# Optimization experiments

Measured on AMD Instinct MI355X. Metric: run time of the kernel, lower is better.

The kernel has to match this reference:

```python
import jax, jax.numpy as jnp
import numpy as np

N_NODES = 100000
IN_DIM = 128
HIDDEN = 64
N_EDGES = 1600000


def setup_inputs() -> dict:
    key = jax.random.key(0)
    k_z, k_e, k_w1, k_b1, k_w2, k_b2 = jax.random.split(key, 6)
    z = jax.random.normal(k_z, (N_NODES, IN_DIM), dtype=jnp.float32)
    edge_index = jax.random.randint(k_e, (2, N_EDGES), 0, N_NODES, dtype=jnp.int64)
    # PyTorch Linear stores weight [out, in]; keep [in, out] layout for x @ W
    bound1 = 1.0 / np.sqrt(2 * IN_DIM)
    W1 = jax.random.uniform(k_w1, (2 * IN_DIM, HIDDEN), jnp.float32, -bound1, bound1)
    b1 = jax.random.uniform(k_b1, (HIDDEN,), jnp.float32, -bound1, bound1)
    bound2 = 1.0 / np.sqrt(HIDDEN)
    W2 = jax.random.uniform(k_w2, (HIDDEN, 1), jnp.float32, -bound2, bound2)
    b2 = jax.random.uniform(k_b2, (1,), jnp.float32, -bound2, bound2)
    return {"z": z, "edge_index": edge_index, "W1": W1, "b1": b1, "W2": W2, "b2": b2}


def reference(z, edge_index, W1, b1, W2, b2):
    src = edge_index[0]
    dst = edge_index[1]
    # gather node features and concat: [E, 2*D]
    edge_feat = jnp.concatenate([z[src], z[dst]], axis=-1)
    h = jax.nn.relu(edge_feat @ W1 + b1)  # [E, H]
    logits = h @ W2 + b2                  # [E, 1]
    return jax.nn.sigmoid(logits).squeeze(-1)  # [E]
```

## Files before the change

kernel.cpp:

```cpp
#include <hip/hip_runtime.h>
#include <hip/hip_bf16.h>

#define N_NODES 100000
#define IN_DIM  128
#define HIDDEN  64
#define N_EDGES 1600000

typedef unsigned short u16;
typedef unsigned int   u32;

typedef __attribute__((ext_vector_type(8))) short bf16x8;
typedef __attribute__((ext_vector_type(4))) float f32x4;

__device__ __forceinline__ u16 f2bf(float f) {
    u32 u = __float_as_uint(f);
    u32 r = 0x7FFFu + ((u >> 16) & 1u);
    u += r;
    return (u16)(u >> 16);
}

__global__ __launch_bounds__(256) void prep_kernel(const float* __restrict__ W1,
                                                   u16* __restrict__ WcatT) {
    int idx = blockIdx.x * 256 + threadIdx.x;
    int jj = idx >> 7;
    int k  = idx & 127;
    float v = (jj < 64) ? W1[k * 64 + jj] : W1[(128 + k) * 64 + (jj - 64)];
    WcatT[idx] = f2bf(v);
}

#define LDK 136
#define GEMM_BLOCKS 625

__global__ __launch_bounds__(256) void gemm_kernel(const float* __restrict__ z,
                                                   const u16* __restrict__ WcatT,
                                                   const float* __restrict__ b1,
                                                   u16* __restrict__ UV) {
    __shared__ u16 Bs[128 * LDK];

    int tid = threadIdx.x;
    for (int c = tid; c < 128 * 16; c += 256) {
        int row = c >> 4, cc = c & 15;
        *(uint4*)(Bs + row * LDK + cc * 8) = *(const uint4*)(WcatT + row * 128 + cc * 8);
    }
    __syncthreads();

    int wave = tid >> 6;
    int lane = tid & 63;
    int quad = lane >> 4;
    int l16  = lane & 15;

    int gwid   = blockIdx.x * 4 + wave;
    int nwaves = GEMM_BLOCKS * 4;
    const int NTILES = N_NODES / 16;

    float bias[4];
#pragma unroll
    for (int nt = 0; nt < 4; nt++) bias[nt] = b1[nt * 16 + l16];

    for (int t = gwid; t < NTILES; t += nwaves) {
        const float* zrow = z + (size_t)(t * 16 + l16) * 128;

        float4 fa[8];
#pragma unroll
        for (int kb = 0; kb < 4; kb++) {
            fa[kb * 2]     = *(const float4*)(zrow + kb * 32 + quad * 8);
            fa[kb * 2 + 1] = *(const float4*)(zrow + kb * 32 + quad * 8 + 4);
        }
        bf16x8 afrag[4];
#pragma unroll
        for (int kb = 0; kb < 4; kb++) {
            union { bf16x8 v; u32 w[4]; } pk;
            float4 lo = fa[kb * 2], hi = fa[kb * 2 + 1];
            pk.w[0] = (u32)f2bf(lo.x) | ((u32)f2bf(lo.y) << 16);
            pk.w[1] = (u32)f2bf(lo.z) | ((u32)f2bf(lo.w) << 16);
            pk.w[2] = (u32)f2bf(hi.x) | ((u32)f2bf(hi.y) << 16);
            pk.w[3] = (u32)f2bf(hi.z) | ((u32)f2bf(hi.w) << 16);
            afrag[kb] = pk.v;
        }

        f32x4 acc[8];
        const f32x4 z4 = {0.f, 0.f, 0.f, 0.f};
#pragma unroll
        for (int i = 0; i < 8; i++) acc[i] = z4;

#pragma unroll
        for (int kb = 0; kb < 4; kb++) {
            int k0 = kb * 32 + quad * 8;
#pragma unroll
            for (int nt = 0; nt < 8; nt++) {
                bf16x8 b = *(const bf16x8*)(Bs + (nt * 16 + l16) * LDK + k0);
                acc[nt] = __builtin_amdgcn_mfma_f32_16x16x32_bf16(afrag[kb], b, acc[nt], 0, 0, 0);
            }
        }

#pragma unroll
        for (int nt = 0; nt < 8; nt++) {
            float bb = (nt < 4) ? bias[nt] : 0.f;
#pragma unroll
            for (int r = 0; r < 4; r++) {
                int row = t * 16 + quad * 4 + r;
                UV[(size_t)row * 128 + nt * 16 + l16] = f2bf(acc[nt][r] + bb);
            }
        }
    }
}

#define EDGE_ITERS 8
#define BATCH 4

__global__ __launch_bounds__(256) void edge_kernel(const int* __restrict__ ei,
                                                   const u16* __restrict__ UV,
                                                   const float* __restrict__ W2,
                                                   const float* __restrict__ b2,
                                                   float* __restrict__ out) {
    int gwave = (blockIdx.x * 256 + threadIdx.x) >> 6;
    int lane  = threadIdx.x & 63;
    int sub   = lane >> 3;
    int c     = lane & 7;

    float4 w2a = *(const float4*)(W2 + c * 8);
    float4 w2b = *(const float4*)(W2 + c * 8 + 4);
    float w2r[8] = {w2a.x, w2a.y, w2a.z, w2a.w, w2b.x, w2b.y, w2b.z, w2b.w};
    float b2v = b2[0];

    int ebase = gwave * (8 * EDGE_ITERS) + sub;

#pragma unroll
    for (int it4 = 0; it4 < EDGE_ITERS; it4 += BATCH) {
        int sB[BATCH], dB[BATCH];
#pragma unroll
        for (int j = 0; j < BATCH; j++) {
            int e = ebase + (it4 + j) * 8;
            sB[j] = ei[e];
            dB[j] = ei[N_EDGES + e];
        }
        uint4 aB[BATCH], bB[BATCH];
#pragma unroll
        for (int j = 0; j < BATCH; j++) {
            aB[j] = *(const uint4*)(UV + (size_t)sB[j] * 128 + c * 8);
            bB[j] = *(const uint4*)(UV + (size_t)dB[j] * 128 + 64 + c * 8);
        }
#pragma unroll
        for (int j = 0; j < BATCH; j++) {
            u32 aw[4] = {aB[j].x, aB[j].y, aB[j].z, aB[j].w};
            u32 bw[4] = {bB[j].x, bB[j].y, bB[j].z, bB[j].w};
            float acc = 0.f;
#pragma unroll
            for (int i = 0; i < 4; i++) {
                float u0 = __uint_as_float(aw[i] << 16);
                float u1 = __uint_as_float(aw[i] & 0xFFFF0000u);
                float v0 = __uint_as_float(bw[i] << 16);
                float v1 = __uint_as_float(bw[i] & 0xFFFF0000u);
                float h0 = fmaxf(u0 + v0, 0.f);
                float h1 = fmaxf(u1 + v1, 0.f);
                acc = fmaf(h0, w2r[i * 2], acc);
                acc = fmaf(h1, w2r[i * 2 + 1], acc);
            }
            acc += __shfl_xor(acc, 1);
            acc += __shfl_xor(acc, 2);
            acc += __shfl_xor(acc, 4);
            if (c == 0) {
                int e = ebase + (it4 + j) * 8;
                float x = acc + b2v;
                out[e] = 1.f / (1.f + __expf(-x));
            }
        }
    }
}

extern "C" void kernel_launch(void* const* d_in, const int* in_sizes, int n_in,
                              void* d_out, int out_size, void* d_ws, size_t ws_size,
                              hipStream_t stream) {
    const float* z  = (const float*)d_in[0];
    const int*   ei = (const int*)d_in[1];
    const float* W1 = (const float*)d_in[2];
    const float* b1 = (const float*)d_in[3];
    const float* W2 = (const float*)d_in[4];
    const float* b2 = (const float*)d_in[5];
    float* out = (float*)d_out;

    u16* WcatT = (u16*)d_ws;
    u16* UV    = (u16*)((char*)d_ws + 65536);

    prep_kernel<<<64, 256, 0, stream>>>(W1, WcatT);
    gemm_kernel<<<GEMM_BLOCKS, 256, 0, stream>>>(z, WcatT, b1, UV);
    edge_kernel<<<6250, 256, 0, stream>>>(ei, UV, W2, b2, out);
}
```

Baseline: 164.2 us.

## Store per-node projections as FP8 and batch all edge gathers up front

The GEMM now writes the projected node features U/V as FP8 (e4m3 via hardware pack conversion) instead of bf16. This halves the intermediate buffer and the random-gather traffic in the edge kernel. The edge kernel issues all 8 edges' index and feature loads before computing, with a scheduling barrier, nontemporal index loads and stores, and a launch-bounds occupancy hint. FP8 quantization adds noticeable error in the hidden activations, which could exceed the accuracy tolerance.

After: 151.6 us. 7.7% less time.

```diff
diff --git a/kernel.cpp b/kernel.cpp
--- a/kernel.cpp
+++ b/kernel.cpp
@@ -8,15 +8,22 @@
 
 typedef unsigned short u16;
 typedef unsigned int   u32;
+typedef unsigned char  u8;
 
 typedef __attribute__((ext_vector_type(8))) short bf16x8;
 typedef __attribute__((ext_vector_type(4))) float f32x4;
+typedef __attribute__((ext_vector_type(2))) float f32x2;
 
 __device__ __forceinline__ u16 f2bf(float f) {
     u32 u = __float_as_uint(f);
     u32 r = 0x7FFFu + ((u >> 16) & 1u);
     u += r;
     return (u16)(u >> 16);
+}
+
+__device__ __forceinline__ u8 f2fp8(float f) {
+    u32 p = (u32)__builtin_amdgcn_cvt_pk_fp8_f32(f, f, 0, false);
+    return (u8)(p & 0xFF);
 }
 
 __global__ __launch_bounds__(256) void prep_kernel(const float* __restrict__ W1,
@@ -34,7 +41,7 @@
 __global__ __launch_bounds__(256) void gemm_kernel(const float* __restrict__ z,
                                                    const u16* __restrict__ WcatT,
                                                    const float* __restrict__ b1,
-                                                   u16* __restrict__ UV) {
+                                                   u8* __restrict__ UVq) {
     __shared__ u16 Bs[128 * LDK];
 
     int tid = threadIdx.x;
@@ -99,20 +106,19 @@
 #pragma unroll
             for (int r = 0; r < 4; r++) {
                 int row = t * 16 + quad * 4 + r;
-                UV[(size_t)row * 128 + nt * 16 + l16] = f2bf(acc[nt][r] + bb);
+                UVq[(size_t)row * 128 + nt * 16 + l16] = f2fp8(acc[nt][r] + bb);
             }
         }
     }
 }
 
-#define EDGE_ITERS 8
-#define BATCH 4
+#define BATCH 8
 
-__global__ __launch_bounds__(256) void edge_kernel(const int* __restrict__ ei,
-                                                   const u16* __restrict__ UV,
-                                                   const float* __restrict__ W2,
-                                                   const float* __restrict__ b2,
-                                                   float* __restrict__ out) {
+__global__ __launch_bounds__(256, 2) void edge_kernel(const int* __restrict__ ei,
+                                                      const u8* __restrict__ UVq,
+                                                      const float* __restrict__ W2,
+                                                      const float* __restrict__ b2,
+                                                      float* __restrict__ out) {
     int gwave = (blockIdx.x * 256 + threadIdx.x) >> 6;
     int lane  = threadIdx.x & 63;
     int sub   = lane >> 3;
@@ -123,47 +129,49 @@
     float w2r[8] = {w2a.x, w2a.y, w2a.z, w2a.w, w2b.x, w2b.y, w2b.z, w2b.w};
     float b2v = b2[0];
 
-    int ebase = gwave * (8 * EDGE_ITERS) + sub;
+    int ebase = gwave * 64 + sub;
+
+    int sB[BATCH], dB[BATCH];
+#pragma unroll
+    for (int j = 0; j < BATCH; j++) {
+        int e = ebase + j * 8;
+        sB[j] = __builtin_nontemporal_load(ei + e);
+        dB[j] = __builtin_nontemporal_load(ei + N_EDGES + e);
+    }
+    uint2 aB[BATCH], bB[BATCH];
+#pragma unroll
+    for (int j = 0; j < BATCH; j++) {
+        aB[j] = *(const uint2*)(UVq + (size_t)sB[j] * 128 + c * 8);
+        bB[j] = *(const uint2*)(UVq + (size_t)dB[j] * 128 + 64 + c * 8);
+    }
+    __builtin_amdgcn_sched_barrier(0);
 
 #pragma unroll
-    for (int it4 = 0; it4 < EDGE_ITERS; it4 += BATCH) {
-        int sB[BATCH], dB[BATCH];
+    for (int j = 0; j < BATCH; j++) {
+        u32 aw[2] = {aB[j].x, aB[j].y};
+        u32 bw[2] = {bB[j].x, bB[j].y};
+        float acc = 0.f;
 #pragma unroll
-        for (int j = 0; j < BATCH; j++) {
-            int e = ebase + (it4 + j) * 8;
-            sB[j] = ei[e];
-            dB[j] = ei[N_EDGES + e];
+        for (int i = 0; i < 2; i++) {
+            f32x2 uu0 = __builtin_amdgcn_cvt_pk_f32_fp8(aw[i], false);
+            f32x2 vv0 = __builtin_amdgcn_cvt_pk_f32_fp8(bw[i], false);
+            f32x2 uu1 = __builtin_amdgcn_cvt_pk_f32_fp8(aw[i], true);
+            f32x2 vv1 = __builtin_amdgcn_cvt_pk_f32_fp8(bw[i], true);
+            float h0 = fmaxf(uu0.x + vv0.x, 0.f);
+            float h1 = fmaxf(uu0.y + vv0.y, 0.f);
+            float h2 = fmaxf(uu1.x + vv1.x, 0.f);
+            float h3 = fmaxf(uu1.y + vv1.y, 0.f);
+            acc = fmaf(h0, w2r[i * 4 + 0], acc);
+            acc = fmaf(h1, w2r[i * 4 + 1], acc);
+            acc = fmaf(h2, w2r[i * 4 + 2], acc);
+            acc = fmaf(h3, w2r[i * 4 + 3], acc);
         }
-        uint4 aB[BATCH], bB[BATCH];
-#pragma unroll
-        for (int j = 0; j < BATCH; j++) {
-            aB[j] = *(const uint4*)(UV + (size_t)sB[j] * 128 + c * 8);
-            bB[j] = *(const uint4*)(UV + (size_t)dB[j] * 128 + 64 + c * 8);
-        }
-#pragma unroll
-        for (int j = 0; j < BATCH; j++) {
-            u32 aw[4] = {aB[j].x, aB[j].y, aB[j].z, aB[j].w};
-            u32 bw[4] = {bB[j].x, bB[j].y, bB[j].z, bB[j].w};
-            float acc = 0.f;
-#pragma unroll
-            for (int i = 0; i < 4; i++) {
-                float u0 = __uint_as_float(aw[i] << 16);
-                float u1 = __uint_as_float(aw[i] & 0xFFFF0000u);
-                float v0 = __uint_as_float(bw[i] << 16);
-                float v1 = __uint_as_float(bw[i] & 0xFFFF0000u);
-                float h0 = fmaxf(u0 + v0, 0.f);
-                float h1 = fmaxf(u1 + v1, 0.f);
-                acc = fmaf(h0, w2r[i * 2], acc);
-                acc = fmaf(h1, w2r[i * 2 + 1], acc);
-            }
-            acc += __shfl_xor(acc, 1);
-            acc += __shfl_xor(acc, 2);
-            acc += __shfl_xor(acc, 4);
-            if (c == 0) {
-                int e = ebase + (it4 + j) * 8;
-                float x = acc + b2v;
-                out[e] = 1.f / (1.f + __expf(-x));
-            }
+        acc += __shfl_xor(acc, 1);
+        acc += __shfl_xor(acc, 2);
+        acc += __shfl_xor(acc, 4);
+        if (c == 0) {
+            float x = acc + b2v;
+            __builtin_nontemporal_store(1.f / (1.f + __expf(-x)), out + ebase + j * 8);
         }
     }
 }
@@ -180,9 +188,9 @@
     float* out = (float*)d_out;
 
     u16* WcatT = (u16*)d_ws;
-    u16* UV    = (u16*)((char*)d_ws + 65536);
+    u8*  UVq   = (u8*)((char*)d_ws + 65536);
 
     prep_kernel<<<64, 256, 0, stream>>>(W1, WcatT);
-    gemm_kernel<<<GEMM_BLOCKS, 256, 0, stream>>>(z, WcatT, b1, UV);
-    edge_kernel<<<6250, 256, 0, stream>>>(ei, UV, W2, b2, out);
+    gemm_kernel<<<GEMM_BLOCKS, 256, 0, stream>>>(z, WcatT, b1, UVq);
+    edge_kernel<<<6250, 256, 0, stream>>>(ei, UVq, W2, b2, out);
 }
```
